# Kernel tuning notes

Measured on AMD Instinct MI355X. Metric: run time of the kernel, lower is better.

## Reference

```python
import jax, jax.numpy as jnp
from jax import lax
import numpy as np

B, T = 32, 15
THR1, THR2 = 15.0, 10.0  # conv1_t, conv2_t


def _conv(x, w):
    # x: (B,T,C,H,W) cumulative potentials/spikes; conv applied per timestep
    b, t, c, h, wd = x.shape
    y = lax.conv_general_dilated(x.reshape(b * t, c, h, wd), w, (1, 1), 'VALID',
                                 dimension_numbers=('NCHW', 'OIHW', 'NCHW'))
    return y.reshape(b, t, *y.shape[1:])


def _pool(x, k, s):
    b, t, c, h, wd = x.shape
    y = lax.reduce_window(x.reshape(b * t, c, h, wd), -jnp.inf, lax.max,
                          (1, 1, k, k), (1, 1, s, s), 'VALID')
    return y.reshape(b, t, *y.shape[1:])


def _pad(x, p):
    return jnp.pad(x, ((0, 0), (0, 0), (0, 0), (p, p), (p, p)))


def _fire(pot, thr):
    # sf.fire: F.threshold_(pot, thr, 0); spk = sign
    th = jnp.where(pot > thr, pot, 0.0)
    return jnp.sign(th), th


def _winner_class(pot, spk):
    # sf.get_k_winners(pot, kwta=1, r=0, spk): earliest spike, tie-break by potential
    b, t = spk.shape[:2]
    cnt = spk.sum(axis=1)                                   # (B,F,H,W) spike counts
    first = jnp.clip((t - cnt).astype(jnp.int32), 0, t - 1)  # earliest spike time
    vals = jnp.take_along_axis(pot, first[:, None], axis=1)[:, 0]  # pot at spike time
    trunc = spk * vals[:, None]                              # (B,T,F,H,W)
    v = trunc.reshape(b, -1).max(axis=1) * t                 # dominance offset per sample
    total = (trunc + spk * v[:, None, None, None, None]).sum(axis=1)  # (B,F,H,W)
    flat = total.reshape(b, -1)
    idx = jnp.argmax(flat, axis=1)
    mx = jnp.max(flat, axis=1)
    hw = pot.shape[-1] * pot.shape[-2]
    feat = idx // hw
    # decision_map: 10 classes x 20 features each -> class = feat // 20; -1 if no spike
    return jnp.where(mx != 0, feat // 20, -1).astype(jnp.int32)


def setup_inputs() -> dict:
    key = jax.random.key(0)
    k1, k2, k3, k4 = jax.random.split(key, 4)
    # cumulative binary spike wave: neuron fires at t_fire and stays 1 afterwards
    t_fire = jax.random.randint(k1, (B, 18, 32, 32), 0, T + 1)
    inp = (jnp.arange(T)[None, :, None, None, None] >= t_fire[:, None]).astype(jnp.float32)
    w1 = 0.8 + 0.05 * jax.random.normal(k2, (90, 18, 7, 7), dtype=jnp.float32)
    w2 = 0.8 + 0.05 * jax.random.normal(k3, (250, 90, 5, 5), dtype=jnp.float32)
    w3 = 0.8 + 0.05 * jax.random.normal(k4, (200, 250, 5, 5), dtype=jnp.float32)
    return {'input': inp, 'w1': w1, 'w2': w2, 'w3': w3, 'max_layer': 3}


def reference(input, w1, w2, w3, max_layer):
    # eval-mode forward of CIFAR10Net
    x = _pad(input, 2)                       # (B,T,18,36,36)
    spk1, pot1 = _fire(_conv(x, w1), THR1)   # (B,T,90,30,30)
    if max_layer == 1:
        return spk1, pot1
    spk2, pot2 = _fire(_conv(_pad(_pool(spk1, 2, 2), 1), w2), THR2)  # (B,T,250,13,13)
    if max_layer == 2:
        return spk2, pot2
    pot3 = _conv(_pad(_pool(spk2, 3, 3), 2), w3)   # (B,T,200,4,4)
    t = pot3.shape[1]
    mask = (jnp.arange(t) == t - 1).astype(pot3.dtype)[None, :, None, None, None]
    spk3 = jnp.sign(pot3 * mask)             # fire with threshold=None: only last step
    cls = _winner_class(pot3, spk3)          # (B,) predicted class or -1
    return cls, pot3
```

## Files before the change

kernel.cpp:

```cpp
#include <hip/hip_runtime.h>

#define NB 32
#define NT 15


__device__ __forceinline__ float gather8(const int* lst, int i, const char* wb) {
    int4 p0 = *(const int4*)(lst + i);
    int4 p1 = *(const int4*)(lst + i + 4);
    int o0 = __builtin_amdgcn_readfirstlane(p0.x);
    int o1 = __builtin_amdgcn_readfirstlane(p0.y);
    int o2 = __builtin_amdgcn_readfirstlane(p0.z);
    int o3 = __builtin_amdgcn_readfirstlane(p0.w);
    int o4 = __builtin_amdgcn_readfirstlane(p1.x);
    int o5 = __builtin_amdgcn_readfirstlane(p1.y);
    int o6 = __builtin_amdgcn_readfirstlane(p1.z);
    int o7 = __builtin_amdgcn_readfirstlane(p1.w);
    float a0 = *(const float*)(wb + o0);
    float a1 = *(const float*)(wb + o1);
    float a2 = *(const float*)(wb + o2);
    float a3 = *(const float*)(wb + o3);
    float a4 = *(const float*)(wb + o4);
    float a5 = *(const float*)(wb + o5);
    float a6 = *(const float*)(wb + o6);
    float a7 = *(const float*)(wb + o7);
    return ((a0 + a1) + (a2 + a3)) + ((a4 + a5) + (a6 + a7));
}

__device__ __forceinline__ void tr_tile(const float* __restrict__ src, float* __restrict__ dst,
                                        int F, int K, int KK, int CIN, int nkt, int t, int tid) {
    __shared__ float lds[32][33];
    int kt = t % nkt, ft = t / nkt;
    int k0 = kt * 32, f0 = ft * 32;
    int tx = tid & 31, ty = tid >> 5;
#pragma unroll
    for (int i = 0; i < 4; i++) {
        int fl = ty + 8 * i;
        int f = f0 + fl, k = k0 + tx;
        lds[fl][tx] = (f < F && k < K) ? src[(size_t)f * K + k] : 0.f;
    }
    __syncthreads();
#pragma unroll
    for (int i = 0; i < 4; i++) {
        int row = ty + 8 * i;
        int k = k0 + row, f = f0 + tx;
        if (k < K && f < F) {
            int j = (k % KK) * CIN + k / KK;
            dst[(size_t)j * F + f] = lds[tx][row];
        }
    }
}

__global__ __launch_bounds__(256) void k_pre(const float* __restrict__ inp,
                                             const float* __restrict__ w1,
                                             const float* __restrict__ w2,
                                             const float* __restrict__ w3,
                                             float* __restrict__ wT1, float* __restrict__ wT2,
                                             float* __restrict__ wT3,
                                             float* __restrict__ PosS2, float* __restrict__ PosS3,
                                             unsigned char* __restrict__ ft1,
                                             unsigned char* __restrict__ nzc1,
                                             int* __restrict__ lcnt, int* __restrict__ list1) {
    int blk = blockIdx.x, tid = threadIdx.x;
    if (blk < 2024) {
        const float* src; float* dst;
        int F, K, KK, CIN, nkt, t;
        if (blk < 84)       { src = w1; dst = wT1; F = 90;  K = 882;  KK = 49; CIN = 18;  nkt = 28;  t = blk; }
        else if (blk < 652) { src = w2; dst = wT2; F = 250; K = 2250; KK = 25; CIN = 90;  nkt = 71;  t = blk - 84; }
        else                { src = w3; dst = wT3; F = 200; K = 6250; KK = 25; CIN = 250; nkt = 196; t = blk - 652; }
        tr_tile(src, dst, F, K, KK, CIN, nkt, t, tid);
    } else if (blk == 2024) {
        if (tid < 90)  wT1[882 * 90 + tid] = 0.f;
        if (tid < 250) wT2[(size_t)2250 * 250 + tid] = 0.f;
        if (tid < 200) wT3[(size_t)6250 * 200 + tid] = 0.f;
    } else if (blk < 2050) {
        int idx = (blk - 2025) * 256 + tid;
        if (idx < 6250) {
            int f = idx / 25, pos = idx - f * 25;
            float acc = 0.f;
#pragma unroll 9
            for (int c = 0; c < 90; c++) acc += w2[(size_t)(f * 90 + c) * 25 + pos];
            PosS2[pos * 256 + f] = acc;
        }
    } else if (blk < 2070) {
        int idx = (blk - 2050) * 256 + tid;
        if (idx < 5000) {
            int f = idx / 25, pos = idx - f * 25;
            float acc = 0.f;
#pragma unroll 10
            for (int c = 0; c < 250; c++) acc += w3[(size_t)(f * 250 + c) * 25 + pos];
            PosS3[pos * 200 + f] = acc;
        }
    } else if (blk < 2703) {
        int i = (blk - 2070) * 256 + tid;
        if (i < 162000) ((uint4*)ft1)[i] = uint4{0, 0, 0, 0};
    } else if (blk < 2712) {
        int i = (blk - 2703) * 256 + tid;
        if (i < 2143) ((uint4*)nzc1)[i] = uint4{0, 0, 0, 0};
    } else {
        int b = blk - 2712;
        __shared__ unsigned char zl[36][36];
        __shared__ unsigned short rs[36][30];
        __shared__ float wm4[4];
        __shared__ float m1s;
        __shared__ int lc;
        for (int i = tid; i < 1296; i += 256) ((unsigned char*)zl)[i] = 0;
        if (tid == 0) lc = 0;
        __syncthreads();
#pragma unroll
        for (int k = 0; k < 4; k++) {
            int pix = tid + k * 256;
            int y = pix >> 5, x = pix & 31;
            const float* p = inp + (size_t)b * 276480 + y * 32 + x;
            int z = 0;
#pragma unroll
            for (int c = 0; c < 18; c++) z += (p[(size_t)c * 1024] != 0.f);
            zl[y + 2][x + 2] = (unsigned char)z;
        }
        float m = 1e30f;
        const float4* w4 = (const float4*)w1;
        for (int i = tid; i < 19845; i += 256) {
            float4 v = w4[i];
            m = fminf(m, fminf(fminf(v.x, v.y), fminf(v.z, v.w)));
        }
        for (int o = 32; o > 0; o >>= 1) m = fminf(m, __shfl_down(m, o));
        if ((tid & 63) == 0) wm4[tid >> 6] = m;
        __syncthreads();
        if (tid == 0) m1s = fminf(fminf(wm4[0], wm4[1]), fminf(wm4[2], wm4[3]));
        __syncthreads();
        for (int i = tid; i < 1080; i += 256) {
            int y = i / 30, x = i - (i / 30) * 30;
            int s = 0;
#pragma unroll
            for (int d = 0; d < 7; d++) s += zl[y][x + d];
            rs[y][x] = (unsigned short)s;
        }
        __syncthreads();
        float m1 = m1s;
        for (int i = tid; i < 900; i += 256) {
            int oy = i / 30, ox = i - (i / 30) * 30;
            int s = 0;
#pragma unroll
            for (int d = 0; d < 7; d++) s += rs[oy + d][ox];
            if (!((float)s * m1 > 15.0f)) {
                int pos = atomicAdd(&lc, 1);
                list1[b * 900 + pos] = b * 900 + i;
            }
        }
        __syncthreads();
        if (tid == 0) lcnt[b] = lc;
    }
}

__global__ __launch_bounds__(256) void k_conv1(const float* __restrict__ inp,
                                               const float* __restrict__ wT1,
                                               const float* __restrict__ PosS2,
                                               const float* __restrict__ PosS3,
                                               const int* __restrict__ lcnt,
                                               const int* __restrict__ list1,
                                               unsigned char* __restrict__ ft1,
                                               unsigned char* __restrict__ nzc1,
                                               unsigned char* __restrict__ nzb1,
                                               float* __restrict__ W2e,
                                               unsigned char* __restrict__ ft2,
                                               unsigned char* __restrict__ nzc2,
                                               int* __restrict__ nzg2,
                                               float* __restrict__ W3s) {
    __shared__ __align__(16) int slist[896];
    __shared__ int scnt, spcnt;
    __shared__ int sbase[33];
    int blk = blockIdx.x, tid = threadIdx.x;
    if (blk < 512) {
        if (tid == 0) {
            int n = 0;
#pragma unroll
            for (int b = 0; b < NB; b++) { sbase[b] = n; n += lcnt[b]; }
            sbase[NB] = n;
        }
        __syncthreads();
        int n1 = sbase[NB];
        for (int it = blk; it < n1; it += 512) {
            __syncthreads();
            int sb = 0;
            while (sb < NB - 1 && it >= sbase[sb + 1]) sb++;
            int idx = list1[sb * 900 + (it - sbase[sb])];
            int b = idx / 900, p = idx - b * 900;
            int oy = p / 30, ox = p - oy * 30;
            unsigned char myft[4];
#pragma unroll
            for (int k = 0; k < 4; k++) {
                int j = tid + k * 256;
                unsigned char v = 255;
                if (j < 882) {
                    int dy = j / 126, rem = j - dy * 126;
                    int dx = rem / 18, c = rem - dx * 18;
                    int y = oy + dy - 2, x = ox + dx - 2;
                    v = 15;
                    if ((unsigned)y < 32u && (unsigned)x < 32u)
                        v = (inp[(size_t)b * 276480 + (size_t)c * 1024 + y * 32 + x] != 0.f) ? 0 : 200;
                }
                myft[k] = v;
            }
            int f = tid < 90 ? tid : 89;
            const char* wb = (const char*)(wT1 + f);
            const int zoff = 882 * 90 * 4;
            float acc = 0.f; int ftv = 15;
            for (int s = 0; s < 15; s++) {
                if (s == 1) {
#pragma unroll
                    for (int k = 0; k < 4; k++) {
                        if (myft[k] == 200) {
                            int j = tid + k * 256;
                            int dy = j / 126, rem = j - dy * 126;
                            int dx = rem / 18, c = rem - dx * 18;
                            int y = oy + dy - 2, x = ox + dx - 2;
                            const float* q = inp + (size_t)b * 276480 + (size_t)c * 1024 + y * 32 + x;
                            int cf = 0;
#pragma unroll
                            for (int t = 1; t < NT; t++) cf += (q[(size_t)t * 18432] != 0.f);
                            myft[k] = (unsigned char)(15 - cf);
                        }
                    }
                }
                if (tid == 0) scnt = 0;
                __syncthreads();
#pragma unroll
                for (int k = 0; k < 4; k++) {
                    if ((int)myft[k] == s) { int pp = atomicAdd(&scnt, 1); slist[pp] = (tid + k * 256) * 360; }
                }
                __syncthreads();
                if (tid == 0) {
                    int c0 = scnt, cp = (c0 + 7) & ~7;
                    for (int i = c0; i < cp; i++) slist[i] = zoff;
                    spcnt = cp;
                }
                __syncthreads();
                int e = spcnt;
                for (int i = 0; i < e; i += 8) acc += gather8(slist, i, wb);
                if (ftv == 15 && acc > 15.0f) ftv = s;
                if (__syncthreads_and(ftv != 15)) break;
            }
            if (tid < 90) {
                ft1[(size_t)idx * 90 + tid] = (unsigned char)ftv;
                if (ftv != 0) { nzc1[idx] = 1; nzb1[b] = 1; }
            }
            __syncthreads();
        }
    } else if (blk < 681) {
        int p = blk - 512;
        int oy = p / 13, ox = p - oy * 13;
        int f = tid < 250 ? tid : 249;
        float W = 0.f;
#pragma unroll
        for (int pos = 0; pos < 25; pos++) {
            int r = pos / 5, x = pos - r * 5;
            int gy = oy + r, gx = ox + x;
            if (!(gy == 0 || gy == 16 || gx == 0 || gx == 16)) W += PosS2[pos * 256 + f];
        }
        if (tid < 250) W2e[p * 256 + tid] = W;
        unsigned char v = (W > 10.0f) ? 0 : 15;
        if (tid < 250)
            for (int b = 0; b < NB; b++) ft2[(size_t)(b * 169 + p) * 250 + tid] = v;
        int nz = (tid < 250 && W <= 10.0f) ? 1 : 0;
        int any = __syncthreads_or(nz);
        if (tid < NB) nzc2[tid * 169 + p] = (unsigned char)any;
        if (tid == 0 && any) *nzg2 = 1;
    } else {
        int px = blk - 681;
        int f = tid < 200 ? tid : 199;
        int oy = px >> 2, ox = px & 3;
        int r0 = max(0, 2 - oy), r1 = min(4, 5 - oy);
        int x0 = max(0, 2 - ox), x1 = min(4, 5 - ox);
        float s = 0.f;
        for (int r = r0; r <= r1; r++)
            for (int x = x0; x <= x1; x++) s += PosS3[(r * 5 + x) * 200 + f];
        if (tid < 200) W3s[px * 200 + tid] = s;
    }
}

__global__ __launch_bounds__(256) void k_conv2(const unsigned char* __restrict__ ft1,
                                               const unsigned char* __restrict__ nzc1,
                                               const unsigned char* __restrict__ nzb1,
                                               const float* __restrict__ wT2,
                                               const float* __restrict__ W2e,
                                               const float* __restrict__ W3s,
                                               unsigned char* __restrict__ ft2,
                                               unsigned char* __restrict__ nzc2,
                                               unsigned char* __restrict__ nzb2,
                                               float* __restrict__ out) {
    constexpr int PADCAP = 2250 + 15 * 8;
    __shared__ __align__(16) int perm[PADCAP];
    __shared__ int start[16], cur[16];
    __shared__ int cntCs, anynz;
    int blk = blockIdx.x, tid = threadIdx.x;
    if (blk >= 5408) {
        int i = (blk - 5408) * 256 + tid;
        int g = i * 4;
        int px0 = g & 15;
        int f = (g >> 4) % 200;
        float4 v;
        v.x = W3s[(px0 + 0) * 200 + f];
        v.y = W3s[(px0 + 1) * 200 + f];
        v.z = W3s[(px0 + 2) * 200 + f];
        v.w = W3s[(px0 + 3) * 200 + f];
        *(float4*)(out + 32 + (size_t)g) = v;
        return;
    }
    int idx = blk;
    int b = idx / 169, p = idx - b * 169;
    if (nzb1[b] == 0) return;
    int oy = p / 13, ox = p - oy * 13;
    int gy0 = max(1, oy), gy1 = min(15, oy + 4);
    int gx0 = max(1, ox), gx1 = min(15, ox + 4);
    int y0 = 2 * (gy0 - 1), y1 = 2 * (gy1 - 1) + 1;
    int x0 = 2 * (gx0 - 1), x1 = 2 * (gx1 - 1) + 1;
    int Wd = x1 - x0 + 1, cells = (y1 - y0 + 1) * Wd;
    const unsigned char* nb = nzc1 + b * 900;
    int v = 0;
    if (tid < cells) { int yy = y0 + tid / Wd, xx = x0 + tid % Wd; v = nb[yy * 30 + xx]; }
    int dirty = __syncthreads_or(v);
    if (!dirty) return;
    const unsigned char* fb = ft1 + (size_t)b * 81000;
    if (tid == 0) { cntCs = 0; anynz = 0; }
    if (tid < 16) cur[tid] = 0;
    unsigned char myft[9];
    int nc = 0;
#pragma unroll
    for (int k = 0; k < 9; k++) {
        int j = tid + k * 256;
        myft[k] = 0;
        if (j < 2250) {
            int r = j / 450, rem = j - r * 450;
            int x = rem / 90, c = rem - x * 90;
            int gy = oy + r, gx = ox + x;
            if (gy >= 1 && gy <= 15 && gx >= 1 && gx <= 15) {
                const unsigned char* q = fb + ((size_t)((gy - 1) * 2) * 30 + (gx - 1) * 2) * 90 + c;
                int m = q[0];
                m = min(m, (int)q[90]);
                m = min(m, (int)q[2700]);
                m = min(m, (int)q[2790]);
                myft[k] = (unsigned char)m;
            }
        }
        nc += (myft[k] >= 1);
    }
    for (int o = 32; o > 0; o >>= 1) nc += __shfl_down(nc, o);
    __syncthreads();
    if ((tid & 63) == 0) atomicAdd(&cntCs, nc);
    __syncthreads();
    int f = tid < 250 ? tid : 249;
    float W = W2e[p * 256 + f];
    int ftv;
    if (cntCs == 0) {
        ftv = (W > 10.0f) ? 0 : 15;
    } else {
#pragma unroll
        for (int k = 0; k < 9; k++) { int vv = myft[k]; if (vv >= 1) atomicAdd(&cur[vv - 1], 1); }
        __syncthreads();
        if (tid == 0) {
            int s = 0;
#pragma unroll
            for (int j = 0; j < 15; j++) { int c = cur[j]; start[j] = s; s += (c + 7) & ~7; }
            start[15] = s;
        }
        __syncthreads();
        int nnzp = start[15];
        if (tid < 15) cur[tid] = start[tid];
        const int zoff = 2250 * 250 * 4;
        for (int i = tid; i < nnzp; i += 256) perm[i] = zoff;
        __syncthreads();
#pragma unroll
        for (int k = 0; k < 9; k++) {
            int vv = myft[k];
            if (vv >= 1) { int pp = atomicAdd(&cur[vv - 1], 1); perm[pp] = (tid + k * 256) * 1000; }
        }
        __syncthreads();
        const char* wb = (const char*)(wT2 + f);
        float R = 0.f; int ft = 15;
        for (int j = 14; j >= 0; j--) {
            int sjb = start[j], e = start[j + 1];
            for (int i = sjb; i < e; i += 8) R += gather8(perm, i, wb);
            float pot = W - R;
            if (pot > 10.0f) ft = j;
            if (sjb == 0) { if (pot > 10.0f) ft = 0; break; }
            if (__all(pot <= 10.0f)) break;
        }
        ftv = ft;
    }
    if (tid < 250) {
        ft2[(size_t)idx * 250 + tid] = (unsigned char)ftv;
        if (ftv != 0) anynz = 1;
    }
    __syncthreads();
    if (tid == 0) {
        nzc2[idx] = (unsigned char)(anynz ? 1 : 0);
        if (anynz) nzb2[b] = 1;
    }
}

__global__ __launch_bounds__(256) void k_conv3w(const unsigned char* __restrict__ ft2,
                                                const unsigned char* __restrict__ nzc2,
                                                const unsigned char* __restrict__ nzb2,
                                                const int* __restrict__ nzg2,
                                                const float* __restrict__ wT3,
                                                const float* __restrict__ W3s,
                                                float* __restrict__ out) {
    constexpr int PADCAP = 4000 + 15 * 8;
    __shared__ __align__(16) int perm[PADCAP];
    __shared__ int start[16], cur[16];
    __shared__ int fbs[16], rowb[16];
    __shared__ float sv[256];
    __shared__ int   si[256];
    int b = blockIdx.x, tid = threadIdx.x;
    int maybe = nzg2[0] | (int)nzb2[b];
    if (maybe) {
        for (int p = 0; p < 16; p++) {
            int oy = p >> 2, ox = p & 3;
            int r0 = max(0, 2 - oy), r1 = min(4, 5 - oy);
            int x0 = max(0, 2 - ox), x1 = min(4, 5 - ox);
            int py0 = oy + r0 - 2, py1 = oy + r1 - 2;
            int qx0 = ox + x0 - 2, qx1 = ox + x1 - 2;
            int sy0 = 3 * py0, sy1 = 3 * py1 + 2;
            int sx0 = 3 * qx0, sx1 = 3 * qx1 + 2;
            int Wd = sx1 - sx0 + 1, cells = (sy1 - sy0 + 1) * Wd;
            const unsigned char* nb2 = nzc2 + b * 169;
            int v = 0;
            if (tid < cells) { int yy = sy0 + tid / Wd, xx = sx0 + tid % Wd; v = nb2[yy * 13 + xx]; }
            int dirty = __syncthreads_or(v);
            if (!dirty) continue;
            int VR = r1 - r0 + 1, VC = x1 - x0 + 1;
            int NP = VR * VC, NV = NP * 250;
            const unsigned char* fb = ft2 + (size_t)b * 42250;
            if (tid < NP) {
                int rv = tid / VC, xv = tid - rv * VC;
                int py = oy + r0 + rv - 2, pxx = ox + x0 + xv - 2;
                fbs[tid]  = (py * 3 * 13 + pxx * 3) * 250;
                rowb[tid] = ((r0 + rv) * 5 + (x0 + xv)) * 250;
            }
            if (tid < 16) cur[tid] = 0;
            __syncthreads();
            unsigned char myft[16];
#pragma unroll
            for (int k = 0; k < 16; k++) {
                int i = tid + k * 256;
                myft[k] = 0;
                if (i < NV) {
                    int posv = i / 250, c = i - posv * 250;
                    const unsigned char* q = fb + fbs[posv] + c;
                    int m = q[0];
#pragma unroll
                    for (int dy = 0; dy < 3; dy++)
#pragma unroll
                        for (int dx = 0; dx < 3; dx++)
                            if (dy | dx) m = min(m, (int)q[(dy * 13 + dx) * 250]);
                    myft[k] = (unsigned char)m;
                }
            }
#pragma unroll
            for (int k = 0; k < 16; k++) { int vv = myft[k]; if (vv >= 1) atomicAdd(&cur[vv - 1], 1); }
            __syncthreads();
            if (tid == 0) {
                int s = 0;
#pragma unroll
                for (int j = 0; j < 15; j++) { int c = cur[j]; start[j] = s; s += (c + 7) & ~7; }
                start[15] = s;
            }
            __syncthreads();
            int nnzp = start[15];
            if (tid < 15) cur[tid] = start[tid];
            const int zoff = 6250 * 200 * 4;
            for (int i = tid; i < nnzp; i += 256) perm[i] = zoff;
            __syncthreads();
#pragma unroll
            for (int k = 0; k < 16; k++) {
                int vv = myft[k];
                if (vv >= 1) {
                    int i = tid + k * 256;
                    int posv = i / 250, c = i - posv * 250;
                    int pp = atomicAdd(&cur[vv - 1], 1);
                    perm[pp] = (rowb[posv] + c) * 800;
                }
            }
            __syncthreads();

            int f = tid < 200 ? tid : 199;
            const char* wb = (const char*)(wT3 + f);
            float W = W3s[p * 200 + f];
            float* o = out + 32 + ((size_t)b * NT) * 3200 + f * 16 + p;
            float R = 0.f;
            for (int j = 14; j >= 0; j--) {
                int sjb = start[j], e = start[j + 1];
                for (int i = sjb; i < e; i += 8) R += gather8(perm, i, wb);
                float pot = W - R;
                if (tid < 200) o[(size_t)j * 3200] = pot;
                if (sjb == 0) {
                    for (int jj = j - 1; jj >= 0; jj--)
                        if (tid < 200) o[(size_t)jj * 3200] = pot;
                    break;
                }
            }
            __syncthreads();
        }
    }
    __syncthreads();
    const float* p14 = out + 32 + ((size_t)b * NT + 14) * 3200;
    float m = 0.f;
    for (int j = tid; j < 3200; j += 256) {
        float v = p14[j];
        if (v > 0.f && v > m) m = v;
    }
    sv[tid] = m;
    __syncthreads();
    for (int s = 128; s > 0; s >>= 1) {
        if (tid < s) sv[tid] = fmaxf(sv[tid], sv[tid + s]);
        __syncthreads();
    }
    float vofs = 15.f * sv[0];
    __syncthreads();
    float bestv = 0.f; int besti = 0x3fffffff;
    for (int j = tid; j < 3200; j += 256) {
        float v = p14[j];
        float tot = (v > 0.f) ? v + vofs : 0.f;
        if (tot > bestv) { bestv = tot; besti = j; }
    }
    sv[tid] = bestv; si[tid] = besti;
    __syncthreads();
    for (int s = 128; s > 0; s >>= 1) {
        if (tid < s) {
            if (sv[tid + s] > sv[tid] || (sv[tid + s] == sv[tid] && si[tid + s] < si[tid])) {
                sv[tid] = sv[tid + s]; si[tid] = si[tid + s];
            }
        }
        __syncthreads();
    }
    if (tid == 0) {
        float mx = sv[0];
        int cls = (mx != 0.f) ? ((si[0] / 16) / 20) : -1;
        out[b] = (float)cls;
    }
}

extern "C" void kernel_launch(void* const* d_in, const int* in_sizes, int n_in,
                              void* d_out, int out_size, void* d_ws, size_t ws_size,
                              hipStream_t stream) {
    const float* inp = (const float*)d_in[0];
    const float* w1  = (const float*)d_in[1];
    const float* w2  = (const float*)d_in[2];
    const float* w3  = (const float*)d_in[3];
    float* out = (float*)d_out;

    unsigned char* ws   = (unsigned char*)d_ws;
    unsigned char* ft1  = ws + 0;
    unsigned char* ft2  = ws + 2592000;
    float* wT1   = (float*)(ws + 3944000);
    float* wT2   = (float*)(ws + 4261888);
    float* wT3   = (float*)(ws + 6512896);
    float* PosS2 = (float*)(ws + 11513728);
    float* PosS3 = (float*)(ws + 11539328);
    float* W2e   = (float*)(ws + 11559328);
    float* W3s   = (float*)(ws + 11732384);
    unsigned char* nzc1 = ws + 11786912;
    unsigned char* nzc2 = ws + 11815712;
    unsigned char* nzb1 = ws + 11821120;
    unsigned char* nzb2 = ws + 11821152;
    int* nzg2  = (int*)(ws + 11821184);
    int* lcnt  = (int*)(ws + 11821200);
    int* list1 = (int*)(ws + 11821440);

    hipLaunchKernelGGL(k_pre, dim3(2744), dim3(256), 0, stream,
                       inp, w1, w2, w3, wT1, wT2, wT3, PosS2, PosS3, ft1, nzc1, lcnt, list1);
    hipLaunchKernelGGL(k_conv1, dim3(697), dim3(256), 0, stream,
                       inp, wT1, PosS2, PosS3, lcnt, list1, ft1, nzc1, nzb1, W2e, ft2, nzc2, nzg2, W3s);
    hipLaunchKernelGGL(k_conv2, dim3(6908), dim3(256), 0, stream,
                       ft1, nzc1, nzb1, wT2, W2e, W3s, ft2, nzc2, nzb2, out);
    hipLaunchKernelGGL(k_conv3w, dim3(NB), dim3(256), 0, stream,
                       ft2, nzc2, nzb2, nzg2, wT3, W3s, out);
}
```

Before: 140.6 us.

## Drop weight transposes and gather directly from original OIHW weight layout

Removes the per-call transpose of all three weight tensors in the prep kernel, so the conv kernels gather from the original weights. Offsets are recomputed into OIHW order, and each thread now reads with a per-filter stride instead of reading contiguous filters across a wavefront. Zero-padding of the sparse lists is replaced by a tail gather that handles a partial group of fewer than eight entries. This saves the transpose traffic and a launch-size chunk of blocks, but the weight gathers become uncoalesced across lanes, which may raise memory cost in the hot conv loops.

```diff
diff --git a/kernel.cpp b/kernel.cpp
--- a/kernel.cpp
+++ b/kernel.cpp
@@ -26,54 +26,31 @@
     return ((a0 + a1) + (a2 + a3)) + ((a4 + a5) + (a6 + a7));
 }
 
-__device__ __forceinline__ void tr_tile(const float* __restrict__ src, float* __restrict__ dst,
-                                        int F, int K, int KK, int CIN, int nkt, int t, int tid) {
-    __shared__ float lds[32][33];
-    int kt = t % nkt, ft = t / nkt;
-    int k0 = kt * 32, f0 = ft * 32;
-    int tx = tid & 31, ty = tid >> 5;
-#pragma unroll
-    for (int i = 0; i < 4; i++) {
-        int fl = ty + 8 * i;
-        int f = f0 + fl, k = k0 + tx;
-        lds[fl][tx] = (f < F && k < K) ? src[(size_t)f * K + k] : 0.f;
-    }
-    __syncthreads();
-#pragma unroll
-    for (int i = 0; i < 4; i++) {
-        int row = ty + 8 * i;
-        int k = k0 + row, f = f0 + tx;
-        if (k < K && f < F) {
-            int j = (k % KK) * CIN + k / KK;
-            dst[(size_t)j * F + f] = lds[tx][row];
-        }
-    }
+__device__ __forceinline__ float gatherN(const int* lst, int i, int n, const char* wb) {
+    float a[8];
+#pragma unroll
+    for (int k = 0; k < 8; k++) {
+        float v = 0.f;
+        if (k < n) {
+            int o = __builtin_amdgcn_readfirstlane(lst[i + k]);
+            v = *(const float*)(wb + o);
+        }
+        a[k] = v;
+    }
+    return ((a[0] + a[1]) + (a[2] + a[3])) + ((a[4] + a[5]) + (a[6] + a[7]));
 }
 
 __global__ __launch_bounds__(256) void k_pre(const float* __restrict__ inp,
                                              const float* __restrict__ w1,
                                              const float* __restrict__ w2,
                                              const float* __restrict__ w3,
-                                             float* __restrict__ wT1, float* __restrict__ wT2,
-                                             float* __restrict__ wT3,
                                              float* __restrict__ PosS2, float* __restrict__ PosS3,
                                              unsigned char* __restrict__ ft1,
                                              unsigned char* __restrict__ nzc1,
                                              int* __restrict__ lcnt, int* __restrict__ list1) {
     int blk = blockIdx.x, tid = threadIdx.x;
-    if (blk < 2024) {
-        const float* src; float* dst;
-        int F, K, KK, CIN, nkt, t;
-        if (blk < 84)       { src = w1; dst = wT1; F = 90;  K = 882;  KK = 49; CIN = 18;  nkt = 28;  t = blk; }
-        else if (blk < 652) { src = w2; dst = wT2; F = 250; K = 2250; KK = 25; CIN = 90;  nkt = 71;  t = blk - 84; }
-        else                { src = w3; dst = wT3; F = 200; K = 6250; KK = 25; CIN = 250; nkt = 196; t = blk - 652; }
-        tr_tile(src, dst, F, K, KK, CIN, nkt, t, tid);
-    } else if (blk == 2024) {
-        if (tid < 90)  wT1[882 * 90 + tid] = 0.f;
-        if (tid < 250) wT2[(size_t)2250 * 250 + tid] = 0.f;
-        if (tid < 200) wT3[(size_t)6250 * 200 + tid] = 0.f;
-    } else if (blk < 2050) {
-        int idx = (blk - 2025) * 256 + tid;
+    if (blk < 25) {
+        int idx = blk * 256 + tid;
         if (idx < 6250) {
             int f = idx / 25, pos = idx - f * 25;
             float acc = 0.f;
@@ -81,8 +58,8 @@
             for (int c = 0; c < 90; c++) acc += w2[(size_t)(f * 90 + c) * 25 + pos];
             PosS2[pos * 256 + f] = acc;
         }
-    } else if (blk < 2070) {
-        int idx = (blk - 2050) * 256 + tid;
+    } else if (blk < 45) {
+        int idx = (blk - 25) * 256 + tid;
         if (idx < 5000) {
             int f = idx / 25, pos = idx - f * 25;
             float acc = 0.f;
@@ -90,14 +67,14 @@
             for (int c = 0; c < 250; c++) acc += w3[(size_t)(f * 250 + c) * 25 + pos];
             PosS3[pos * 200 + f] = acc;
         }
-    } else if (blk < 2703) {
-        int i = (blk - 2070) * 256 + tid;
+    } else if (blk < 678) {
+        int i = (blk - 45) * 256 + tid;
         if (i < 162000) ((uint4*)ft1)[i] = uint4{0, 0, 0, 0};
-    } else if (blk < 2712) {
-        int i = (blk - 2703) * 256 + tid;
+    } else if (blk < 687) {
+        int i = (blk - 678) * 256 + tid;
         if (i < 2143) ((uint4*)nzc1)[i] = uint4{0, 0, 0, 0};
     } else {
-        int b = blk - 2712;
+        int b = blk - 687;
         __shared__ unsigned char zl[36][36];
         __shared__ unsigned short rs[36][30];
         __shared__ float wm4[4];
@@ -152,7 +129,7 @@
 }
 
 __global__ __launch_bounds__(256) void k_conv1(const float* __restrict__ inp,
-                                               const float* __restrict__ wT1,
+                                               const float* __restrict__ w1,
                                                const float* __restrict__ PosS2,
                                                const float* __restrict__ PosS3,
                                                const int* __restrict__ lcnt,
@@ -166,7 +143,7 @@
                                                int* __restrict__ nzg2,
                                                float* __restrict__ W3s) {
     __shared__ __align__(16) int slist[896];
-    __shared__ int scnt, spcnt;
+    __shared__ int scnt;
     __shared__ int sbase[33];
     int blk = blockIdx.x, tid = threadIdx.x;
     if (blk < 512) {
@@ -201,8 +178,7 @@
                 myft[k] = v;
             }
             int f = tid < 90 ? tid : 89;
-            const char* wb = (const char*)(wT1 + f);
-            const int zoff = 882 * 90 * 4;
+            const char* wb = (const char*)(w1 + (size_t)f * 882);
             float acc = 0.f; int ftv = 15;
             for (int s = 0; s < 15; s++) {
                 if (s == 1) {
@@ -225,17 +201,20 @@
                 __syncthreads();
 #pragma unroll
                 for (int k = 0; k < 4; k++) {
-                    if ((int)myft[k] == s) { int pp = atomicAdd(&scnt, 1); slist[pp] = (tid + k * 256) * 360; }
+                    if ((int)myft[k] == s) {
+                        int j = tid + k * 256;
+                        int dy = j / 126, rem = j - dy * 126;
+                        int dx = rem / 18, c = rem - dx * 18;
+                        int pp = atomicAdd(&scnt, 1);
+                        slist[pp] = (c * 49 + dy * 7 + dx) * 4;
+                    }
                 }
                 __syncthreads();
-                if (tid == 0) {
-                    int c0 = scnt, cp = (c0 + 7) & ~7;
-                    for (int i = c0; i < cp; i++) slist[i] = zoff;
-                    spcnt = cp;
-                }
-                __syncthreads();
-                int e = spcnt;
-                for (int i = 0; i < e; i += 8) acc += gather8(slist, i, wb);
+                int c0 = scnt;
+                int full = c0 & ~7;
+                for (int i = 0; i < full; i += 8) acc += gather8(slist, i, wb);
+                int nt = c0 - full;
+                if (nt) acc += gatherN(slist, full, nt, wb);
                 if (ftv == 15 && acc > 15.0f) ftv = s;
                 if (__syncthreads_and(ftv != 15)) break;
             }
@@ -280,7 +259,7 @@
 __global__ __launch_bounds__(256) void k_conv2(const unsigned char* __restrict__ ft1,
                                                const unsigned char* __restrict__ nzc1,
                                                const unsigned char* __restrict__ nzb1,
-                                               const float* __restrict__ wT2,
+                                               const float* __restrict__ w2,
                                                const float* __restrict__ W2e,
                                                const float* __restrict__ W3s,
                                                unsigned char* __restrict__ ft2,
@@ -289,7 +268,7 @@
                                                float* __restrict__ out) {
     constexpr int PADCAP = 2250 + 15 * 8;
     __shared__ __align__(16) int perm[PADCAP];
-    __shared__ int start[16], cur[16];
+    __shared__ int start[16], cur[16], rcnt[15];
     __shared__ int cntCs, anynz;
     int blk = blockIdx.x, tid = threadIdx.x;
     if (blk >= 5408) {
@@ -356,6 +335,7 @@
 #pragma unroll
         for (int k = 0; k < 9; k++) { int vv = myft[k]; if (vv >= 1) atomicAdd(&cur[vv - 1], 1); }
         __syncthreads();
+        if (tid < 15) rcnt[tid] = cur[tid];
         if (tid == 0) {
             int s = 0;
 #pragma unroll
@@ -363,22 +343,30 @@
             start[15] = s;
         }
         __syncthreads();
-        int nnzp = start[15];
         if (tid < 15) cur[tid] = start[tid];
-        const int zoff = 2250 * 250 * 4;
-        for (int i = tid; i < nnzp; i += 256) perm[i] = zoff;
         __syncthreads();
 #pragma unroll
         for (int k = 0; k < 9; k++) {
             int vv = myft[k];
-            if (vv >= 1) { int pp = atomicAdd(&cur[vv - 1], 1); perm[pp] = (tid + k * 256) * 1000; }
-        }
-        __syncthreads();
-        const char* wb = (const char*)(wT2 + f);
+            if (vv >= 1) {
+                int j = tid + k * 256;
+                int r = j / 450, rem = j - r * 450;
+                int x = rem / 90, c = rem - x * 90;
+                int pp = atomicAdd(&cur[vv - 1], 1);
+                perm[pp] = (c * 25 + (r * 5 + x)) * 4;
+            }
+        }
+        __syncthreads();
+        const char* wb = (const char*)(w2 + (size_t)f * 2250);
         float R = 0.f; int ft = 15;
         for (int j = 14; j >= 0; j--) {
-            int sjb = start[j], e = start[j + 1];
-            for (int i = sjb; i < e; i += 8) R += gather8(perm, i, wb);
+            int sjb = start[j];
+            int rc = rcnt[j];
+            int rend = sjb + rc;
+            int i = sjb;
+            for (; i + 8 <= rend; i += 8) R += gather8(perm, i, wb);
+            int nt = rend - i;
+            if (nt > 0) R += gatherN(perm, i, nt, wb);
             float pot = W - R;
             if (pot > 10.0f) ft = j;
             if (sjb == 0) { if (pot > 10.0f) ft = 0; break; }
@@ -401,12 +389,12 @@
                                                 const unsigned char* __restrict__ nzc2,
                                                 const unsigned char* __restrict__ nzb2,
                                                 const int* __restrict__ nzg2,
-                                                const float* __restrict__ wT3,
+                                                const float* __restrict__ w3,
                                                 const float* __restrict__ W3s,
                                                 float* __restrict__ out) {
     constexpr int PADCAP = 4000 + 15 * 8;
     __shared__ __align__(16) int perm[PADCAP];
-    __shared__ int start[16], cur[16];
+    __shared__ int start[16], cur[16], rcnt[15];
     __shared__ int fbs[16], rowb[16];
     __shared__ float sv[256];
     __shared__ int   si[256];
@@ -434,7 +422,7 @@
                 int rv = tid / VC, xv = tid - rv * VC;
                 int py = oy + r0 + rv - 2, pxx = ox + x0 + xv - 2;
                 fbs[tid]  = (py * 3 * 13 + pxx * 3) * 250;
-                rowb[tid] = ((r0 + rv) * 5 + (x0 + xv)) * 250;
+                rowb[tid] = (r0 + rv) * 5 + (x0 + xv);
             }
             if (tid < 16) cur[tid] = 0;
             __syncthreads();
@@ -458,6 +446,7 @@
 #pragma unroll
             for (int k = 0; k < 16; k++) { int vv = myft[k]; if (vv >= 1) atomicAdd(&cur[vv - 1], 1); }
             __syncthreads();
+            if (tid < 15) rcnt[tid] = cur[tid];
             if (tid == 0) {
                 int s = 0;
 #pragma unroll
@@ -465,10 +454,7 @@
                 start[15] = s;
             }
             __syncthreads();
-            int nnzp = start[15];
             if (tid < 15) cur[tid] = start[tid];
-            const int zoff = 6250 * 200 * 4;
-            for (int i = tid; i < nnzp; i += 256) perm[i] = zoff;
             __syncthreads();
 #pragma unroll
             for (int k = 0; k < 16; k++) {
@@ -477,19 +463,24 @@
                     int i = tid + k * 256;
                     int posv = i / 250, c = i - posv * 250;
                     int pp = atomicAdd(&cur[vv - 1], 1);
-                    perm[pp] = (rowb[posv] + c) * 800;
+                    perm[pp] = (c * 25 + rowb[posv]) * 4;
                 }
             }
             __syncthreads();
 
             int f = tid < 200 ? tid : 199;
-            const char* wb = (const char*)(wT3 + f);
+            const char* wb = (const char*)(w3 + (size_t)f * 6250);
             float W = W3s[p * 200 + f];
             float* o = out + 32 + ((size_t)b * NT) * 3200 + f * 16 + p;
             float R = 0.f;
             for (int j = 14; j >= 0; j--) {
-                int sjb = start[j], e = start[j + 1];
-                for (int i = sjb; i < e; i += 8) R += gather8(perm, i, wb);
+                int sjb = start[j];
+                int rc = rcnt[j];
+                int rend = sjb + rc;
+                int i = sjb;
+                for (; i + 8 <= rend; i += 8) R += gather8(perm, i, wb);
+                int nt = rend - i;
+                if (nt > 0) R += gatherN(perm, i, nt, wb);
                 float pot = W - R;
                 if (tid < 200) o[(size_t)j * 3200] = pot;
                 if (sjb == 0) {
@@ -551,9 +542,6 @@
     unsigned char* ws   = (unsigned char*)d_ws;
     unsigned char* ft1  = ws + 0;
     unsigned char* ft2  = ws + 2592000;
-    float* wT1   = (float*)(ws + 3944000);
-    float* wT2   = (float*)(ws + 4261888);
-    float* wT3   = (float*)(ws + 6512896);
     float* PosS2 = (float*)(ws + 11513728);
     float* PosS3 = (float*)(ws + 11539328);
     float* W2e   = (float*)(ws + 11559328);
@@ -566,12 +554,12 @@
     int* lcnt  = (int*)(ws + 11821200);
     int* list1 = (int*)(ws + 11821440);
 
-    hipLaunchKernelGGL(k_pre, dim3(2744), dim3(256), 0, stream,
-                       inp, w1, w2, w3, wT1, wT2, wT3, PosS2, PosS3, ft1, nzc1, lcnt, list1);
+    hipLaunchKernelGGL(k_pre, dim3(719), dim3(256), 0, stream,
+                       inp, w1, w2, w3, PosS2, PosS3, ft1, nzc1, lcnt, list1);
     hipLaunchKernelGGL(k_conv1, dim3(697), dim3(256), 0, stream,
-                       inp, wT1, PosS2, PosS3, lcnt, list1, ft1, nzc1, nzb1, W2e, ft2, nzc2, nzg2, W3s);
+                       inp, w1, PosS2, PosS3, lcnt, list1, ft1, nzc1, nzb1, W2e, ft2, nzc2, nzg2, W3s);
     hipLaunchKernelGGL(k_conv2, dim3(6908), dim3(256), 0, stream,
-                       ft1, nzc1, nzb1, wT2, W2e, W3s, ft2, nzc2, nzb2, out);
+                       ft1, nzc1, nzb1, w2, W2e, W3s, ft2, nzc2, nzb2, out);
     hipLaunchKernelGGL(k_conv3w, dim3(NB), dim3(256), 0, stream,
-                       ft2, nzc2, nzb2, nzg2, wT3, W3s, out);
-}
+                       ft2, nzc2, nzb2, nzg2, w3, W3s, out);
+}
```

Result: faster. 135.1 us (-3.9%).
